# Kernel tuning notes

Measured on AMD Instinct MI355X. Metric: run time of the kernel, lower is better.

## Reference

```python
import jax, jax.numpy as jnp
import numpy as np

B, S, D = 2, 2048, 1024
H, DH = 16, 64  # n_heads, d_head; D == H*DH
OUTPUT_SCALE = 1.0
EPS = 1e-08

def setup_inputs() -> dict:
    key = jax.random.key(0)
    k1, k2, k3 = jax.random.split(key, 3)
    x = jax.random.normal(k1, (B, S, D), dtype=jnp.float32)
    # causal-style mask would also work; use all-True [B,S,S] bool mask (True = attend)
    mask = jnp.tril(jnp.ones((S, S), dtype=bool))[None].repeat(B, axis=0)
    Wqkv = jax.random.normal(k2, (D, 3 * D), dtype=jnp.float32) * (1.0 / np.sqrt(D))
    Wo = jax.random.normal(k3, (D, D), dtype=jnp.float32) * (1.0 / np.sqrt(D))
    tau = jnp.full((H, 1, 1), float(DH) ** 0.5, dtype=jnp.float32)  # learned per-head temperature
    return {"x": x, "mask": mask, "Wqkv": Wqkv, "Wo": Wo, "tau": tau}

def reference(x, mask, Wqkv, Wo, tau):
    b, s, d = x.shape
    qkv = x @ Wqkv                                   # [B,S,3D]
    q, k, v = jnp.split(qkv, 3, axis=-1)
    # [B,S,D] -> [B,H,S,DH]
    q = q.reshape(b, s, H, DH).transpose(0, 2, 1, 3)
    k = k.reshape(b, s, H, DH).transpose(0, 2, 1, 3)
    v = v.reshape(b, s, H, DH).transpose(0, 2, 1, 3)
    # L2 normalize Q and K along head dim
    q = q / (jnp.linalg.norm(q, axis=-1, keepdims=True) + EPS)
    k = k / (jnp.linalg.norm(k, axis=-1, keepdims=True) + EPS)
    q = q * tau                                       # per-head learned temperature [H,1,1]
    logits = jnp.einsum('bhqd,bhkd->bhqk', q, k) / jnp.sqrt(jnp.float32(DH))
    m = mask if mask.ndim == 4 else mask[:, None, :, :]
    logits = jnp.where(m, logits, jnp.finfo(logits.dtype).min)
    w = jax.nn.softmax(logits, axis=-1)
    attn = jnp.einsum('bhqk,bhkd->bhqd', w, v)        # [B,H,S,DH]
    attn = attn.transpose(0, 2, 1, 3).reshape(b, s, d)
    return (attn @ Wo) * OUTPUT_SCALE
```

## Files before the change

### kernel.cpp

```cpp
#include <hip/hip_runtime.h>
#include <math.h>

#define BATCH 2
#define SEQ 2048
#define DMODEL 1024
#define NHEAD 16
#define DHEAD 64
#define QKV_COLS (3 * DMODEL)
#define EPS 1e-8f
#define LOG2E 1.44269504f

typedef short bf16x8 __attribute__((ext_vector_type(8)));
typedef float f32x4 __attribute__((ext_vector_type(4)));

static __device__ __forceinline__ unsigned short f2bf(float x) {
  unsigned u = __float_as_uint(x);
  u += 0x7fffu + ((u >> 16) & 1u);
  return (unsigned short)(u >> 16);
}

static __device__ __forceinline__ unsigned cvtpk(float lo, float hi) {
  unsigned r;
  asm("v_cvt_pk_bf16_f32 %0, %1, %2" : "=v"(r) : "v"(lo), "v"(hi));
  return r;
}

static __device__ __forceinline__ void async_ld16(const unsigned short* g,
                                                  unsigned short* l) {
  __builtin_amdgcn_global_load_lds(
      (const __attribute__((address_space(1))) void*)g,
      (__attribute__((address_space(3))) void*)(unsigned int)(unsigned long long)l,
      16, 0, 0);
}

__global__ __launch_bounds__(256) void convert_x_kernel(
    const float* __restrict__ x, unsigned short* __restrict__ xb) {
  const size_t i = ((size_t)blockIdx.x * 256 + threadIdx.x) * 4;
  const float4 a = *(const float4*)(x + i);
  ushort4 r;
  r.x = f2bf(a.x); r.y = f2bf(a.y); r.z = f2bf(a.z); r.w = f2bf(a.w);
  *(ushort4*)(xb + i) = r;
}

__global__ __launch_bounds__(256) void transpose_w2_kernel(
    const float* __restrict__ W0, unsigned short* __restrict__ Wt0,
    const float* __restrict__ W1, unsigned short* __restrict__ Wt1) {
  __shared__ float tile[32][33];
  const int bx = blockIdx.x;
  const float* W;
  unsigned short* Wt;
  int N, n0;
  if (bx < 96) { W = W0; Wt = Wt0; N = QKV_COLS; n0 = bx * 32; }
  else         { W = W1; Wt = Wt1; N = DMODEL;   n0 = (bx - 96) * 32; }
  const int K = DMODEL;
  const int k0 = blockIdx.y * 32;
  const int tx = threadIdx.x, ty = threadIdx.y;
#pragma unroll
  for (int i = 0; i < 4; ++i)
    tile[ty + i * 8][tx] = W[(size_t)(k0 + ty + i * 8) * N + n0 + tx];
  __syncthreads();
#pragma unroll
  for (int i = 0; i < 4; ++i)
    Wt[(size_t)(n0 + ty + i * 8) * K + k0 + tx] = f2bf(tile[tx][ty + i * 8]);
}

__global__ __launch_bounds__(256) void sgemm_bf16_kernel(
    const unsigned short* __restrict__ A, const unsigned short* __restrict__ Bt,
    float* __restrict__ C, int M, int N, int K) {
  __shared__ unsigned short As[2][64 * 32];
  __shared__ unsigned short Bs[2][128 * 32];

  const int t = threadIdx.x;
  const int w = t >> 6;
  const int lane = t & 63;
  const int quad = lane >> 4;
  const int lr = lane & 15;

  const int orig = blockIdx.y * gridDim.x + blockIdx.x;
  const int wg = (orig & 7) * 64 + (orig >> 3);
  const int bx = wg & 7, by = wg >> 3;
  const int m0 = by * 64;
  const int n0 = bx * 128;

  const int srow = lane >> 2;
  const int scol = (lane & 3) * 8;

  auto stage = [&](int k0, int bb) {
#pragma unroll
    for (int ii = 0; ii < 3; ++ii) {
      const int fi = w * 3 + ii;
      if (fi < 4) {
        async_ld16(A + (size_t)(m0 + fi * 16 + srow) * K + k0 + scol,
                   &As[bb][fi * 512]);
      } else {
        const int g = fi - 4;
        async_ld16(Bt + (size_t)(n0 + g * 16 + srow) * K + k0 + scol,
                   &Bs[bb][g * 512]);
      }
    }
  };

  f32x4 acc[4][2];
  const f32x4 zero4 = {0.f, 0.f, 0.f, 0.f};
#pragma unroll
  for (int i = 0; i < 4; ++i)
#pragma unroll
    for (int j = 0; j < 2; ++j) acc[i][j] = zero4;

  stage(0, 0);
  int bb = 0;
  for (int k0 = 0; k0 < K; k0 += 32, bb ^= 1) {
    __syncthreads();
    if (k0 + 32 < K) stage(k0 + 32, bb ^ 1);

    bf16x8 af[4], bfr[2];
#pragma unroll
    for (int i = 0; i < 4; ++i)
      af[i] = *(const bf16x8*)&As[bb][(i * 16 + lr) * 32 + quad * 8];
#pragma unroll
    for (int j = 0; j < 2; ++j)
      bfr[j] = *(const bf16x8*)&Bs[bb][(w * 32 + j * 16 + lr) * 32 + quad * 8];
#pragma unroll
    for (int i = 0; i < 4; ++i)
#pragma unroll
      for (int j = 0; j < 2; ++j)
        acc[i][j] = __builtin_amdgcn_mfma_f32_16x16x32_bf16(af[i], bfr[j], acc[i][j], 0, 0, 0);
  }

#pragma unroll
  for (int i = 0; i < 4; ++i)
#pragma unroll
    for (int r = 0; r < 4; ++r) {
      float* c = C + (size_t)(m0 + i * 16 + quad * 4 + r) * N + n0 + w * 32 + lr;
#pragma unroll
      for (int j = 0; j < 2; ++j) c[j * 16] = acc[i][j][r];
    }
}

__global__ __launch_bounds__(256) void qkv_gemm_norm_kernel(
    const unsigned short* __restrict__ A, const unsigned short* __restrict__ Bt,
    const float* __restrict__ tau,
    unsigned short* __restrict__ Qh, unsigned short* __restrict__ Kh,
    unsigned short* __restrict__ Vh) {
  __shared__ unsigned short As[2][128 * 32];
  __shared__ unsigned short Bs[2][128 * 32];

  const int K = DMODEL;
  const int t = threadIdx.x;
  const int w = t >> 6;
  const int lane = t & 63;
  const int quad = lane >> 4;
  const int lr = lane & 15;
  const int wr = w >> 1, wc = w & 1;

  const int orig = blockIdx.y * gridDim.x + blockIdx.x;
  const int wg = (orig & 7) * 96 + (orig >> 3);
  const int bx = wg % 24, by = wg / 24;
  const int m0 = by * 128;
  const int n0 = bx * 128;

  const int srow = w * 32 + (lane >> 2);
  const int scol = (lane & 3) * 8;
  const unsigned short* ga = A + (size_t)(m0 + srow) * K + scol;
  const unsigned short* gb = Bt + (size_t)(n0 + srow) * K + scol;

  auto stage = [&](int k0, int bb) {
#pragma unroll
    for (int i = 0; i < 2; ++i) {
      async_ld16(ga + (size_t)(i * 16) * K + k0, &As[bb][(w * 32 + i * 16) * 32]);
      async_ld16(gb + (size_t)(i * 16) * K + k0, &Bs[bb][(w * 32 + i * 16) * 32]);
    }
  };

  f32x4 acc[4][4];
  const f32x4 zero4 = {0.f, 0.f, 0.f, 0.f};
#pragma unroll
  for (int i = 0; i < 4; ++i)
#pragma unroll
    for (int j = 0; j < 4; ++j) acc[i][j] = zero4;

  stage(0, 0);
  int bb = 0;
  for (int k0 = 0; k0 < K; k0 += 32, bb ^= 1) {
    __syncthreads();
    if (k0 + 32 < K) stage(k0 + 32, bb ^ 1);

    bf16x8 af[4], bfr[4];
#pragma unroll
    for (int i = 0; i < 4; ++i)
      af[i] = *(const bf16x8*)&As[bb][(wr * 64 + i * 16 + lr) * 32 + quad * 8];
#pragma unroll
    for (int j = 0; j < 4; ++j)
      bfr[j] = *(const bf16x8*)&Bs[bb][(wc * 64 + j * 16 + lr) * 32 + quad * 8];
#pragma unroll
    for (int i = 0; i < 4; ++i)
#pragma unroll
      for (int j = 0; j < 4; ++j)
        acc[i][j] = __builtin_amdgcn_mfma_f32_16x16x32_bf16(af[i], bfr[j], acc[i][j], 0, 0, 0);
  }

  const int col0 = n0 + wc * 64;
  const int which = col0 >> 10;
  const int h = (col0 & 1023) >> 6;
  const float tsc = tau[h] * 0.125f * LOG2E;
  unsigned short* dst = (which == 0) ? Qh : (which == 1) ? Kh : Vh;

#pragma unroll
  for (int i = 0; i < 4; ++i)
#pragma unroll
    for (int r = 0; r < 4; ++r) {
      const int s = m0 + wr * 64 + i * 16 + quad * 4 + r;
      unsigned short* ar =
          dst + (((size_t)((s >> 11) * NHEAD + h)) * SEQ + (s & 2047)) * DHEAD;
      float scale;
      if (which == 2) {
        scale = 1.0f;
      } else {
        float ss = 0.f;
#pragma unroll
        for (int j = 0; j < 4; ++j) ss += acc[i][j][r] * acc[i][j][r];
        ss += __shfl_xor(ss, 1, 16);
        ss += __shfl_xor(ss, 2, 16);
        ss += __shfl_xor(ss, 4, 16);
        ss += __shfl_xor(ss, 8, 16);
        scale = 1.0f / (sqrtf(ss) + EPS);
        if (which == 0) scale *= tsc;
      }
#pragma unroll
      for (int j = 0; j < 4; ++j) ar[j * 16 + lr] = f2bf(acc[i][j][r] * scale);
    }
}

__global__ __launch_bounds__(256) void vtrans_kernel(
    const unsigned short* __restrict__ Vh, unsigned short* __restrict__ Vt) {
  __shared__ unsigned short tile[64][72];
  const int bh = blockIdx.x;
  const int s0 = blockIdx.y * 64;
  const int t = threadIdx.x;
  const int sr = t >> 2;
  const int dc = (t & 3) * 16;
  const unsigned short* src = Vh + ((size_t)bh * SEQ + s0 + sr) * DHEAD + dc;
  *(bf16x8*)&tile[sr][dc]     = *(const bf16x8*)(src);
  *(bf16x8*)&tile[sr][dc + 8] = *(const bf16x8*)(src + 8);
  __syncthreads();
  const int dr = t >> 2;
  const int sc = (t & 3) * 16;
  unsigned short buf[16];
#pragma unroll
  for (int i = 0; i < 16; ++i) buf[i] = tile[sc + i][dr];
  unsigned short* dst = Vt + ((size_t)bh * DHEAD + dr) * SEQ + s0 + sc;
  *(bf16x8*)dst       = *(const bf16x8*)buf;
  *(bf16x8*)(dst + 8) = *(const bf16x8*)(buf + 8);
}

__global__ __launch_bounds__(256, 4) void attn_kernel(
    const unsigned short* __restrict__ Qh, const unsigned short* __restrict__ Kh,
    const unsigned short* __restrict__ Vt, unsigned short* __restrict__ attnb) {
  __shared__ unsigned short Ks[2][64 * 64];
  __shared__ unsigned short Vs[2][64 * 64];

  const int idx = blockIdx.x;
  const int bh = idx & 31;
  const int i2 = idx >> 5;
  const int seg = i2 >> 3, G = i2 & 7;
  const int qb = (seg == 0) ? 31 - G : (seg == 1) ? G : (seg == 2) ? 23 - G : 8 + G;
  const int b = bh >> 4;
  const int h = bh & 15;
  const int t = threadIdx.x;
  const int w = t >> 6;
  const int lane = t & 63;
  const int quad = lane >> 4;
  const int lr = lane & 15;
  const int sw = lr & 7;

  const unsigned short* Qp = Qh + (size_t)bh * SEQ * DHEAD;
  const unsigned short* Kp = Kh + (size_t)bh * SEQ * DHEAD;
  const unsigned short* Vp = Vt + (size_t)bh * DHEAD * SEQ;

  const int rrow = lane >> 3;
  const int swc = ((lane & 7) ^ rrow) * 8;
  const int f0 = w * 4;

  auto stage = [&](int k0, int bb) {
#pragma unroll
    for (int ii = 0; ii < 4; ++ii) {
      const int fi = f0 + ii;
      if (fi < 8) {
        async_ld16(Kp + (size_t)(k0 + fi * 8 + rrow) * DHEAD + swc,
                   &Ks[bb][fi * 512]);
      } else {
        const int g = fi - 8;
        async_ld16(Vp + (size_t)(g * 8 + rrow) * SEQ + k0 + swc,
                   &Vs[bb][g * 512]);
      }
    }
  };

  const f32x4 zero4 = {0.f, 0.f, 0.f, 0.f};
  f32x4 o[4];
  o[0] = o[1] = o[2] = o[3] = zero4;
  f32x4 ol = zero4;

  bf16x8 ones;
#pragma unroll
  for (int i = 0; i < 8; ++i) ones[i] = (short)0x3F80;

  const int q0 = qb * 64 + w * 16;
  const unsigned short* qr = Qp + (size_t)(q0 + lr) * DHEAD;
  const bf16x8 aq0 = *(const bf16x8*)(qr + quad * 8);
  const bf16x8 aq1 = *(const bf16x8*)(qr + 32 + quad * 8);
  const int qrow = q0 + lr;

  const int kend = qb * 64;

  stage(0, 0);
  int bb = 0;

  for (int k0 = 0; k0 <= kend; k0 += 64, bb ^= 1) {
    __syncthreads();
    if (k0 < kend) stage(k0 + 64, bb ^ 1);

    f32x4 c[4];
    __builtin_amdgcn_s_setprio(1);
#pragma unroll
    for (int kt = 0; kt < 4; ++kt) {
      const bf16x8 kf0 =
          *(const bf16x8*)&Ks[bb][(kt * 16 + lr) * 64 + ((quad ^ sw) * 8)];
      const bf16x8 kf1 =
          *(const bf16x8*)&Ks[bb][(kt * 16 + lr) * 64 + (((4 | quad) ^ sw) * 8)];
      f32x4 tt = __builtin_amdgcn_mfma_f32_16x16x32_bf16(kf0, aq0, zero4, 0, 0, 0);
      c[kt] = __builtin_amdgcn_mfma_f32_16x16x32_bf16(kf1, aq1, tt, 0, 0, 0);
    }
    __builtin_amdgcn_s_setprio(0);

    unsigned plo[4], phi[4];
    if (k0 == kend) {
#pragma unroll
      for (int kt = 0; kt < 4; ++kt) {
        float p[4];
#pragma unroll
        for (int r = 0; r < 4; ++r) {
          const int key = k0 + kt * 16 + quad * 4 + r;
          p[r] = (key <= qrow) ? exp2f(c[kt][r]) : 0.f;
        }
        plo[kt] = cvtpk(p[0], p[1]);
        phi[kt] = cvtpk(p[2], p[3]);
      }
    } else {
#pragma unroll
      for (int kt = 0; kt < 4; ++kt) {
        plo[kt] = cvtpk(exp2f(c[kt][0]), exp2f(c[kt][1]));
        phi[kt] = cvtpk(exp2f(c[kt][2]), exp2f(c[kt][3]));
      }
    }

#pragma unroll
    for (int c2 = 0; c2 < 2; ++c2) {
      unsigned aLo = plo[2 * c2],     aHi = phi[2 * c2];
      unsigned bLo = plo[2 * c2 + 1], bHi = phi[2 * c2 + 1];
      asm("v_permlane32_swap_b32 %0, %1" : "+v"(aLo), "+v"(bLo));
      asm("v_permlane32_swap_b32 %0, %1" : "+v"(aHi), "+v"(bHi));
      asm("v_permlane16_swap_b32 %0, %1" : "+v"(aLo), "+v"(bLo));
      asm("v_permlane16_swap_b32 %0, %1" : "+v"(aHi), "+v"(bHi));
      union { unsigned u[4]; bf16x8 v; } pk;
      pk.u[0] = aLo; pk.u[1] = aHi; pk.u[2] = bLo; pk.u[3] = bHi;
      const bf16x8 pa = pk.v;
      __builtin_amdgcn_s_setprio(1);
#pragma unroll
      for (int nt = 0; nt < 4; ++nt) {
        const bf16x8 vb = *(const bf16x8*)&Vs[bb][(nt * 16 + lr) * 64 +
                                                  (((c2 * 4 + quad) ^ sw) * 8)];
        o[nt] = __builtin_amdgcn_mfma_f32_16x16x32_bf16(pa, vb, o[nt], 0, 0, 0);
      }
      ol = __builtin_amdgcn_mfma_f32_16x16x32_bf16(pa, ones, ol, 0, 0, 0);
      __builtin_amdgcn_s_setprio(0);
    }
  }

#pragma unroll
  for (int r = 0; r < 4; ++r) {
    const float invr = 1.0f / ol[r];
    unsigned short* ar =
        attnb + ((size_t)(b * SEQ + q0 + quad * 4 + r)) * DMODEL + h * DHEAD;
#pragma unroll
    for (int nt = 0; nt < 4; ++nt) ar[nt * 16 + lr] = f2bf(o[nt][r] * invr);
  }
}

extern "C" void kernel_launch(void* const* d_in, const int* in_sizes, int n_in,
                              void* d_out, int out_size, void* d_ws, size_t ws_size,
                              hipStream_t stream) {
  const float* x    = (const float*)d_in[0];
  const float* Wqkv = (const float*)d_in[2];
  const float* Wo   = (const float*)d_in[3];
  const float* tau  = (const float*)d_in[4];
  float* out = (float*)d_out;

  unsigned short* attnb = (unsigned short*)d_ws;
  unsigned short* Qh = attnb + (size_t)BATCH * SEQ * DMODEL;
  unsigned short* Kh = Qh + (size_t)BATCH * NHEAD * SEQ * DHEAD;
  unsigned short* Vh = Kh + (size_t)BATCH * NHEAD * SEQ * DHEAD;
  unsigned short* Xb = Vh + (size_t)BATCH * NHEAD * SEQ * DHEAD;
  unsigned short* Wqkv_t = Xb + (size_t)BATCH * SEQ * DMODEL;
  unsigned short* Wo_t = Wqkv_t + (size_t)DMODEL * QKV_COLS;
  unsigned short* Vt = Wo_t + (size_t)DMODEL * DMODEL;

  const int M = BATCH * SEQ;

  convert_x_kernel<<<(M * DMODEL) / (256 * 4), 256, 0, stream>>>(x, Xb);
  transpose_w2_kernel<<<dim3(128, 32), dim3(32, 8), 0, stream>>>(
      Wqkv, Wqkv_t, Wo, Wo_t);

  qkv_gemm_norm_kernel<<<dim3(QKV_COLS / 128, M / 128), 256, 0, stream>>>(
      Xb, Wqkv_t, tau, Qh, Kh, Vh);

  vtrans_kernel<<<dim3(BATCH * NHEAD, SEQ / 64), 256, 0, stream>>>(Vh, Vt);

  attn_kernel<<<dim3(1024), 256, 0, stream>>>(Qh, Kh, Vt, attnb);

  sgemm_bf16_kernel<<<dim3(DMODEL / 128, M / 64), 256, 0, stream>>>(
      attnb, Wo_t, out, M, DMODEL, DMODEL);
}
```

Baseline: 194.4 us.

## Swizzle GEMM LDS tiles and merge prep kernels into one launch

Applies an XOR swizzle to the 16-byte column chunks of the LDS A/B tiles in both bf16 GEMMs, on both the async global-to-LDS stage and the fragment reads, to reduce LDS bank conflicts. The x conversion and the weight transpose kernels are also fused into a single 1D-grid launch to remove one kernel launch. The swizzle adds a little index arithmetic and must keep the store and load mappings consistent.

New measurement: 193.0 us, median of 2. Within noise of the previous version (-0.7%).

```diff
diff --git a/kernel.cpp b/kernel.cpp
--- a/kernel.cpp
+++ b/kernel.cpp
@@ -33,28 +33,30 @@
       16, 0, 0);
 }
 
-__global__ __launch_bounds__(256) void convert_x_kernel(
-    const float* __restrict__ x, unsigned short* __restrict__ xb) {
-  const size_t i = ((size_t)blockIdx.x * 256 + threadIdx.x) * 4;
-  const float4 a = *(const float4*)(x + i);
-  ushort4 r;
-  r.x = f2bf(a.x); r.y = f2bf(a.y); r.z = f2bf(a.z); r.w = f2bf(a.w);
-  *(ushort4*)(xb + i) = r;
-}
-
-__global__ __launch_bounds__(256) void transpose_w2_kernel(
+__global__ __launch_bounds__(256) void prep_kernel(
+    const float* __restrict__ x, unsigned short* __restrict__ xb,
     const float* __restrict__ W0, unsigned short* __restrict__ Wt0,
     const float* __restrict__ W1, unsigned short* __restrict__ Wt1) {
   __shared__ float tile[32][33];
-  const int bx = blockIdx.x;
+  const int bid = blockIdx.x;
+  if (bid < 4096) {
+    const size_t i = ((size_t)bid * 256 + threadIdx.x) * 4;
+    const float4 a = *(const float4*)(x + i);
+    ushort4 r;
+    r.x = f2bf(a.x); r.y = f2bf(a.y); r.z = f2bf(a.z); r.w = f2bf(a.w);
+    *(ushort4*)(xb + i) = r;
+    return;
+  }
+  const int bxx = bid - 4096;
+  const int bxi = bxx & 127;
+  const int k0 = (bxx >> 7) * 32;
   const float* W;
   unsigned short* Wt;
   int N, n0;
-  if (bx < 96) { W = W0; Wt = Wt0; N = QKV_COLS; n0 = bx * 32; }
-  else         { W = W1; Wt = Wt1; N = DMODEL;   n0 = (bx - 96) * 32; }
+  if (bxi < 96) { W = W0; Wt = Wt0; N = QKV_COLS; n0 = bxi * 32; }
+  else          { W = W1; Wt = Wt1; N = DMODEL;   n0 = (bxi - 96) * 32; }
   const int K = DMODEL;
-  const int k0 = blockIdx.y * 32;
-  const int tx = threadIdx.x, ty = threadIdx.y;
+  const int tx = threadIdx.x & 31, ty = threadIdx.x >> 5;
 #pragma unroll
   for (int i = 0; i < 4; ++i)
     tile[ty + i * 8][tx] = W[(size_t)(k0 + ty + i * 8) * N + n0 + tx];
@@ -75,6 +77,7 @@
   const int lane = t & 63;
   const int quad = lane >> 4;
   const int lr = lane & 15;
+  const int rk = (lr >> 1) & 3;
 
   const int orig = blockIdx.y * gridDim.x + blockIdx.x;
   const int wg = (orig & 7) * 64 + (orig >> 3);
@@ -83,7 +86,7 @@
   const int n0 = bx * 128;
 
   const int srow = lane >> 2;
-  const int scol = (lane & 3) * 8;
+  const int scol = ((lane & 3) ^ ((lane >> 3) & 3)) * 8;
 
   auto stage = [&](int k0, int bb) {
 #pragma unroll
@@ -116,10 +119,10 @@
     bf16x8 af[4], bfr[2];
 #pragma unroll
     for (int i = 0; i < 4; ++i)
-      af[i] = *(const bf16x8*)&As[bb][(i * 16 + lr) * 32 + quad * 8];
+      af[i] = *(const bf16x8*)&As[bb][(i * 16 + lr) * 32 + ((quad ^ rk) * 8)];
 #pragma unroll
     for (int j = 0; j < 2; ++j)
-      bfr[j] = *(const bf16x8*)&Bs[bb][(w * 32 + j * 16 + lr) * 32 + quad * 8];
+      bfr[j] = *(const bf16x8*)&Bs[bb][(w * 32 + j * 16 + lr) * 32 + ((quad ^ rk) * 8)];
 #pragma unroll
     for (int i = 0; i < 4; ++i)
 #pragma unroll
@@ -152,6 +155,7 @@
   const int quad = lane >> 4;
   const int lr = lane & 15;
   const int wr = w >> 1, wc = w & 1;
+  const int rk = (lr >> 1) & 3;
 
   const int orig = blockIdx.y * gridDim.x + blockIdx.x;
   const int wg = (orig & 7) * 96 + (orig >> 3);
@@ -160,7 +164,7 @@
   const int n0 = bx * 128;
 
   const int srow = w * 32 + (lane >> 2);
-  const int scol = (lane & 3) * 8;
+  const int scol = ((lane & 3) ^ ((lane >> 3) & 3)) * 8;
   const unsigned short* ga = A + (size_t)(m0 + srow) * K + scol;
   const unsigned short* gb = Bt + (size_t)(n0 + srow) * K + scol;
 
@@ -188,10 +192,10 @@
     bf16x8 af[4], bfr[4];
 #pragma unroll
     for (int i = 0; i < 4; ++i)
-      af[i] = *(const bf16x8*)&As[bb][(wr * 64 + i * 16 + lr) * 32 + quad * 8];
+      af[i] = *(const bf16x8*)&As[bb][(wr * 64 + i * 16 + lr) * 32 + ((quad ^ rk) * 8)];
 #pragma unroll
     for (int j = 0; j < 4; ++j)
-      bfr[j] = *(const bf16x8*)&Bs[bb][(wc * 64 + j * 16 + lr) * 32 + quad * 8];
+      bfr[j] = *(const bf16x8*)&Bs[bb][(wc * 64 + j * 16 + lr) * 32 + ((quad ^ rk) * 8)];
 #pragma unroll
     for (int i = 0; i < 4; ++i)
 #pragma unroll
@@ -407,9 +411,7 @@
 
   const int M = BATCH * SEQ;
 
-  convert_x_kernel<<<(M * DMODEL) / (256 * 4), 256, 0, stream>>>(x, Xb);
-  transpose_w2_kernel<<<dim3(128, 32), dim3(32, 8), 0, stream>>>(
-      Wqkv, Wqkv_t, Wo, Wo_t);
+  prep_kernel<<<dim3(8192), 256, 0, stream>>>(x, Xb, Wqkv, Wqkv_t, Wo, Wo_t);
 
   qkv_gemm_norm_kernel<<<dim3(QKV_COLS / 128, M / 128), 256, 0, stream>>>(
       Xb, Wqkv_t, tau, Qh, Kh, Vh);
```
